# Kernel tuning notes

Hardware: AMD Instinct MI355X
Metric: run time of the kernel (lower is better)

## Reference

```python
import jax, jax.numpy as jnp
import numpy as np

PE_DIM = 64

def _layernorm(x, g, b, eps=1e-5):
    m = jnp.mean(x, -1, keepdims=True)
    v = jnp.mean((x - m) ** 2, -1, keepdims=True)
    return (x - m) * jax.lax.rsqrt(v + eps) * g + b

def _sinusoidal_pe(t, dim=PE_DIM):
    half = dim // 2
    freqs = jnp.exp(-jnp.log(10000.0) * jnp.arange(half) / half).astype(t.dtype)
    ang = t[..., None] * freqs  # [..., half]
    return jnp.concatenate([jnp.sin(ang), jnp.cos(ang)], -1)

def _bilinear(feats, b, t, x, y):
    # feats [B,Wl,H,W,D]; b,t int32 [B,Q,Wl,M] (b broadcastable); x,y in [0,1]
    # matches torch grid_sample(mode=bilinear, padding_mode=border, align_corners=False)
    H, W = feats.shape[2], feats.shape[3]
    px = x * W - 0.5
    py = y * H - 0.5
    x0 = jnp.floor(px); y0 = jnp.floor(py)
    wx = (px - x0)[..., None]; wy = (py - y0)[..., None]
    x0i = jnp.clip(x0.astype(jnp.int32), 0, W - 1)
    x1i = jnp.clip(x0.astype(jnp.int32) + 1, 0, W - 1)
    y0i = jnp.clip(y0.astype(jnp.int32), 0, H - 1)
    y1i = jnp.clip(y0.astype(jnp.int32) + 1, 0, H - 1)
    v00 = feats[b, t, y0i, x0i]  # [B,Q,Wl,M,D]
    v01 = feats[b, t, y0i, x1i]
    v10 = feats[b, t, y1i, x0i]
    v11 = feats[b, t, y1i, x1i]
    return (v00 * (1 - wy) * (1 - wx) + v01 * (1 - wy) * wx
            + v10 * wy * (1 - wx) + v11 * wy * wx)

def setup_inputs() -> dict:
    key = jax.random.key(0)
    ks = jax.random.split(key, 20)
    B, Q, Wl, H, W, D, M = 4, 300, 8, 64, 64, 256, 4
    s = 0.02
    inp = {
        'q': jax.random.normal(ks[0], (B, Q, D), jnp.float32),
        'kv_feats': jax.random.normal(ks[1], (B, Wl, H, W, D), jnp.float32),
        'kv_mask': jnp.zeros((B, Wl, H, W), jnp.bool_),
        'delta_sec': jax.random.normal(ks[2], (B, Q, Wl), jnp.float32),
        'w_ref': jax.random.normal(ks[3], (D, 2), jnp.float32) * s,
        'b_ref': jnp.zeros((2,), jnp.float32),
        'w_delta': jax.random.normal(ks[4], (2 * D, 3 * M), jnp.float32) * s,
        'b_delta': jnp.zeros((3 * M,), jnp.float32),
        'w_alpha': jax.random.normal(ks[5], (2 * D, M), jnp.float32) * s,
        'b_alpha': jnp.zeros((M,), jnp.float32),
        'lam': jnp.array(1.0, jnp.float32),
        'w_proj': jax.random.normal(ks[6], (D, D), jnp.float32) * s,
        'b_proj': jnp.zeros((D,), jnp.float32),
        'ln1_g': jnp.ones((D,), jnp.float32), 'ln1_b': jnp.zeros((D,), jnp.float32),
        'ln2_g': jnp.ones((D,), jnp.float32), 'ln2_b': jnp.zeros((D,), jnp.float32),
        'w_ffn1': jax.random.normal(ks[7], (D, 4 * D), jnp.float32) * s,
        'b_ffn1': jnp.zeros((4 * D,), jnp.float32),
        'w_ffn2': jax.random.normal(ks[8], (4 * D, D), jnp.float32) * s,
        'b_ffn2': jnp.zeros((D,), jnp.float32),
        'w_rel': jax.random.normal(ks[9], (PE_DIM, D), jnp.float32) * s,
        'b_rel': jnp.zeros((D,), jnp.float32),
    }
    return inp

def reference(q, kv_feats, kv_mask, delta_sec, w_ref, b_ref, w_delta, b_delta,
              w_alpha, b_alpha, lam, w_proj, b_proj, ln1_g, ln1_b, ln2_g, ln2_b,
              w_ffn1, b_ffn1, w_ffn2, b_ffn2, w_rel, b_rel):
    B, Q, D = q.shape
    Wl = kv_feats.shape[1]
    M = w_alpha.shape[1]

    qn = _layernorm(q, ln1_g, ln1_b)
    rel_feat = _sinusoidal_pe(delta_sec) @ w_rel + b_rel          # [B,Q,Wl,D]
    psi = jnp.concatenate([jnp.broadcast_to(qn[:, :, None, :], (B, Q, Wl, D)),
                           rel_feat], -1)                          # [B,Q,Wl,2D]

    delta = (psi @ w_delta + b_delta).reshape(B, Q, Wl, M, 3)
    logits = psi @ w_alpha + b_alpha                               # [B,Q,Wl,M]
    ref = jax.nn.sigmoid(qn @ w_ref + b_ref)                       # [B,Q,2]
    coords = ref[:, :, None, None, :] + jnp.tanh(delta[..., :2])   # [B,Q,Wl,M,2]
    coords = jnp.clip(coords, 0.0, 1.0)
    delta_t = jnp.tanh(delta[..., 2])                              # [B,Q,Wl,M]

    # mask features (mask==True -> invalid -> zero)
    feats = kv_feats * (~kv_mask)[..., None].astype(kv_feats.dtype)

    # temporal trilinear indices
    base = jnp.arange(Wl, dtype=q.dtype).reshape(1, 1, Wl, 1)
    target = base + delta_t
    t0f = jnp.clip(jnp.floor(target), 0, Wl - 1)
    t1f = jnp.clip(t0f + 1, 0, Wl - 1)
    alpha = (target - t0f)[..., None]
    t0 = t0f.astype(jnp.int32); t1 = t1f.astype(jnp.int32)

    bidx = jnp.arange(B, dtype=jnp.int32).reshape(B, 1, 1, 1)
    cx = coords[..., 0]; cy = coords[..., 1]
    s0 = _bilinear(feats, bidx, t0, cx, cy)                        # [B,Q,Wl,M,D]
    s1 = _bilinear(feats, bidx, t1, cx, cy)
    sampled = s0 * (1 - alpha) + s1 * alpha

    lam_sp = jax.nn.softplus(lam)
    weights = jax.nn.softmax(logits - lam_sp * jnp.abs(delta_sec)[..., None], axis=-1)
    agg = jnp.sum(weights[..., None] * sampled, axis=(2, 3))       # [B,Q,D]

    out = q + (agg @ w_proj + b_proj)
    h = _layernorm(out, ln2_g, ln2_b)
    ffn = jax.nn.gelu(h @ w_ffn1 + b_ffn1, approximate=False) @ w_ffn2 + b_ffn2
    return out + ffn
```

## Files before the change

### kernel.cpp

```cpp
#include <hip/hip_runtime.h>
#include <math.h>

#define Bn 4
#define Qn 300
#define WL 8
#define Hh 64
#define Ww 64
#define Dd 256
#define Mm 4

__device__ __forceinline__ float wave_reduce(float v) {
#pragma unroll
    for (int off = 32; off > 0; off >>= 1) v += __shfl_down(v, off, 64);
    return v;
}

__device__ __forceinline__ float block_reduce256(float v, float* lds) {
    v = wave_reduce(v);
    int lane = threadIdx.x & 63, wv = threadIdx.x >> 6;
    if (lane == 0) lds[wv] = v;
    __syncthreads();
    float r = lds[0] + lds[1] + lds[2] + lds[3];
    __syncthreads();
    return r;
}

__device__ __forceinline__ float lo16(unsigned u) { return __uint_as_float(u << 16); }
__device__ __forceinline__ float hi16(unsigned u) { return __uint_as_float(u & 0xffff0000u); }

__device__ __forceinline__ unsigned bfp(float a, float b) {
    unsigned ua = __float_as_uint(a); ua = (ua + 0x7fffu + ((ua >> 16) & 1u)) >> 16;
    unsigned ub = __float_as_uint(b); ub = (ub + 0x7fffu + ((ub >> 16) & 1u)) >> 16;
    return ua | (ub << 16);
}

__global__ void __launch_bounds__(256) k_pack(const float* __restrict__ wp,
                                              const float* __restrict__ wf1,
                                              const float* __restrict__ wf2,
                                              unsigned* __restrict__ pk) {
    int i = blockIdx.x * 256 + threadIdx.x;
    if (i < 32768) {
        int kk = i >> 8, c = i & 255;
        pk[i] = bfp(wp[(2 * kk) * 256 + c], wp[(2 * kk + 1) * 256 + c]);
    } else if (i < 163840) {
        int i2 = i - 32768; int kk = i2 >> 10, c = i2 & 1023;
        pk[i] = bfp(wf1[(2 * kk) * 1024 + c], wf1[(2 * kk + 1) * 1024 + c]);
    } else {
        int i3 = i - 163840; int kk = i3 >> 8, c = i3 & 255;
        pk[i] = bfp(wf2[(2 * kk) * 256 + c], wf2[(2 * kk + 1) * 256 + c]);
    }
}

__global__ void __launch_bounds__(256) k_mid(const float* __restrict__ q,
                                             const float* __restrict__ g1,
                                             const float* __restrict__ b1,
                                             const float* __restrict__ w_ref,
                                             const float* __restrict__ b_ref,
                                             const float* __restrict__ dsec,
                                             const float* __restrict__ w_rel,
                                             const float* __restrict__ b_rel,
                                             const float* __restrict__ w_delta,
                                             const float* __restrict__ b_delta,
                                             const float* __restrict__ w_alpha,
                                             const float* __restrict__ b_alpha,
                                             const unsigned char* __restrict__ mask,
                                             unsigned* __restrict__ prm2) {
    __shared__ float lds[4];
    __shared__ float sref[2];
    __shared__ float sqn[256];
    __shared__ float pe[8][64];
    __shared__ float rel[8][260];
    __shared__ float WcT[16 * 516];
    __shared__ float res[8][16];

    int bq = blockIdx.x, t = threadIdx.x;

    float x = q[bq * Dd + t];
    float m = block_reduce256(x, lds) * (1.f / Dd);
    float dx = x - m;
    float v = block_reduce256(dx * dx, lds) * (1.f / Dd);
    float y = dx * rsqrtf(v + 1e-5f) * g1[t] + b1[t];
    sqn[t] = y;

    float s0 = block_reduce256(y * w_ref[t * 2 + 0], lds);
    float s1 = block_reduce256(y * w_ref[t * 2 + 1], lds);
    if (t == 0) {
        sref[0] = 1.f / (1.f + expf(-(s0 + b_ref[0])));
        sref[1] = 1.f / (1.f + expf(-(s1 + b_ref[1])));
    }

    {
        int wl = t >> 5, i = t & 31;
        float f = expf(-logf(10000.f) * (float)i * (1.f / 32.f));
        float a = dsec[bq * WL + wl] * f;
        pe[wl][i] = sinf(a);
        pe[wl][i + 32] = cosf(a);
    }

    for (int u = t; u < 512 * 16; u += 256) {
        int k = u >> 4, jj = u & 15;
        float w = (jj < 12) ? w_delta[k * 12 + jj] : w_alpha[k * 4 + (jj - 12)];
        WcT[jj * 516 + k] = w;
    }

    float wr[64];
#pragma unroll
    for (int k = 0; k < 64; k++) wr[k] = w_rel[k * Dd + t];
    __syncthreads();

    float brl = b_rel[t];
    for (int wl = 0; wl < WL; wl++) {
        const float4* p4 = (const float4*)&pe[wl][0];
        float r = brl;
#pragma unroll
        for (int k4 = 0; k4 < 16; k4++) {
            float4 p = p4[k4];
            r += p.x * wr[4 * k4] + p.y * wr[4 * k4 + 1]
               + p.z * wr[4 * k4 + 2] + p.w * wr[4 * k4 + 3];
        }
        rel[wl][t] = r;
    }
    __syncthreads();

    if (t < 128) {
        int wl = t >> 4, jj = t & 15;
        const float4* wrow = (const float4*)&WcT[jj * 516];
        const float4* qrow = (const float4*)sqn;
        const float4* rrow = (const float4*)&rel[wl][0];
        float s = 0.f;
#pragma unroll 8
        for (int k4 = 0; k4 < 64; k4++) {
            float4 a = qrow[k4], w = wrow[k4];
            s += a.x * w.x + a.y * w.y + a.z * w.z + a.w * w.w;
        }
#pragma unroll 8
        for (int k4 = 0; k4 < 64; k4++) {
            float4 a = rrow[k4], w = wrow[64 + k4];
            s += a.x * w.x + a.y * w.y + a.z * w.z + a.w * w.w;
        }
        s += (jj < 12) ? b_delta[jj] : b_alpha[jj - 12];
        res[wl][jj] = s;
    }
    __syncthreads();

    if (t < 32) {
        int wl = t >> 2, mm = t & 3;
        float l0 = res[wl][12], l1 = res[wl][13], l2 = res[wl][14], l3 = res[wl][15];
        float mx = fmaxf(fmaxf(l0, l1), fmaxf(l2, l3));
        float inv = 1.f / (expf(l0 - mx) + expf(l1 - mx) + expf(l2 - mx) + expf(l3 - mx));
        float wgt = expf(res[wl][12 + mm] - mx) * inv;

        float cx = fminf(fmaxf(sref[0] + tanhf(res[wl][mm * 3 + 0]), 0.f), 1.f);
        float cy = fminf(fmaxf(sref[1] + tanhf(res[wl][mm * 3 + 1]), 0.f), 1.f);
        float tgt = (float)wl + tanhf(res[wl][mm * 3 + 2]);
        float t0f = fminf(fmaxf(floorf(tgt), 0.f), (float)(WL - 1));
        float t1f = fminf(t0f + 1.f, (float)(WL - 1));
        float alpha = tgt - t0f;
        float px = cx * (float)Ww - 0.5f, py = cy * (float)Hh - 0.5f;
        float fx = floorf(px), fy = floorf(py);
        float wx = px - fx, wy = py - fy;
        int X0 = (int)fminf(fmaxf(fx, 0.f), (float)(Ww - 1));
        int X1 = (int)fminf(fmaxf(fx + 1.f, 0.f), (float)(Ww - 1));
        int Y0 = (int)fminf(fmaxf(fy, 0.f), (float)(Hh - 1));
        int Y1 = (int)fminf(fmaxf(fy + 1.f, 0.f), (float)(Hh - 1));
        int T0 = (int)t0f, T1 = (int)t1f;

        float w00 = (1.f - wy) * (1.f - wx), w01 = (1.f - wy) * wx;
        float w10 = wy * (1.f - wx), w11 = wy * wx;
        float wt0 = wgt * (1.f - alpha), wt1 = wgt * alpha;

        int b = bq / Qn;
        int base0 = (b * WL + T0) * Hh;
        int base1 = (b * WL + T1) * Hh;
        int i00 = (base0 + Y0) * Ww + X0, i01 = (base0 + Y0) * Ww + X1;
        int i10 = (base0 + Y1) * Ww + X0, i11 = (base0 + Y1) * Ww + X1;
        int j00 = (base1 + Y0) * Ww + X0, j01 = (base1 + Y0) * Ww + X1;
        int j10 = (base1 + Y1) * Ww + X0, j11 = (base1 + Y1) * Ww + X1;

        unsigned* rec = prm2 + (unsigned)(bq * 32 + t) * 16;
        rec[0] = __float_as_uint(wt0 * w00 * (mask[i00] ? 0.f : 1.f));
        rec[1] = __float_as_uint(wt0 * w01 * (mask[i01] ? 0.f : 1.f));
        rec[2] = __float_as_uint(wt0 * w10 * (mask[i10] ? 0.f : 1.f));
        rec[3] = __float_as_uint(wt0 * w11 * (mask[i11] ? 0.f : 1.f));
        rec[4] = __float_as_uint(wt1 * w00 * (mask[j00] ? 0.f : 1.f));
        rec[5] = __float_as_uint(wt1 * w01 * (mask[j01] ? 0.f : 1.f));
        rec[6] = __float_as_uint(wt1 * w10 * (mask[j10] ? 0.f : 1.f));
        rec[7] = __float_as_uint(wt1 * w11 * (mask[j11] ? 0.f : 1.f));
        rec[8] = i00; rec[9] = i01; rec[10] = i10; rec[11] = i11;
        rec[12] = j00; rec[13] = j01; rec[14] = j10; rec[15] = j11;
    }
}

__global__ void __launch_bounds__(512) k_gather(const float* __restrict__ feats,
                                                const unsigned* __restrict__ prm2,
                                                float* __restrict__ agg) {
    __shared__ unsigned P[32 * 16];
    __shared__ float part[8][256];
    int bq = blockIdx.x, t = threadIdx.x;
    int l = t & 63, j = t >> 6;
    P[t] = prm2[(unsigned)bq * 512 + t];
    __syncthreads();
    const float4* f4 = (const float4*)feats;
    float4 acc = {0.f, 0.f, 0.f, 0.f};
#pragma unroll
    for (int p = 0; p < 4; p++) {
        const unsigned* rec = &P[(j * 4 + p) * 16];
#pragma unroll
        for (int cn = 0; cn < 8; cn++) {
            float w = __uint_as_float(rec[cn]);
            size_t idx = rec[8 + cn];
            float4 v = f4[idx * 64 + l];
            acc.x += w * v.x; acc.y += w * v.y; acc.z += w * v.z; acc.w += w * v.w;
        }
    }
    ((float4*)&part[j][0])[l] = acc;
    __syncthreads();
    if (t < 256) {
        float s = part[0][t] + part[1][t] + part[2][t] + part[3][t]
                + part[4][t] + part[5][t] + part[6][t] + part[7][t];
        agg[(size_t)bq * Dd + t] = s;
    }
}

template<int R>
__device__ __forceinline__ void out_body(int row0,
        const float* __restrict__ q, const float* __restrict__ agg,
        const unsigned* __restrict__ pkP, const float* __restrict__ b_proj,
        const float* __restrict__ g2, const float* __restrict__ b2,
        const unsigned* __restrict__ pkF1, const float* __restrict__ b_ffn1,
        const unsigned* __restrict__ pkF2, const float* __restrict__ b_ffn2,
        float* __restrict__ out,
        float* sA, float* sO, float* sH, float* sF, float* sP, float* sRed) {
    int t = threadIdx.x;
    int c = t & 255, j = t >> 8;

    for (int u = t; u < 256 * R; u += 1024) {
        int r = u >> 8, cc = u & 255;
        sA[r * 256 + cc] = agg[(size_t)(row0 + r) * Dd + cc];
    }
    __syncthreads();

    {
        float acc[R];
#pragma unroll
        for (int r = 0; r < R; r++) acc[r] = 0.f;
        const unsigned* wp = pkP + (j * 32) * 256 + c;
#pragma unroll 4
        for (int q4 = 0; q4 < 16; q4++) {
            unsigned u0 = wp[(2 * q4) * 256];
            unsigned u1 = wp[(2 * q4 + 1) * 256];
            float w0 = lo16(u0), w1 = hi16(u0), w2 = lo16(u1), w3 = hi16(u1);
#pragma unroll
            for (int r = 0; r < R; r++) {
                float4 a = ((const float4*)&sA[r * 256 + j * 64])[q4];
                acc[r] += a.x * w0 + a.y * w1 + a.z * w2 + a.w * w3;
            }
        }
#pragma unroll
        for (int r = 0; r < R; r++) sP[(j * 5 + r) * 256 + c] = acc[r];
    }
    __syncthreads();

    for (int u = t; u < 256 * R; u += 1024) {
        int r = u >> 8, cc = u & 255;
        float o = sP[(0 * 5 + r) * 256 + cc] + sP[(1 * 5 + r) * 256 + cc]
                + sP[(2 * 5 + r) * 256 + cc] + sP[(3 * 5 + r) * 256 + cc]
                + q[(size_t)(row0 + r) * Dd + cc] + b_proj[cc];
        sO[r * 256 + cc] = o;
    }
    __syncthreads();

    {
        int wv = t >> 6, l = t & 63;
        if (wv < R) {
            float4 v = ((const float4*)&sO[wv * 256])[l];
            float s = v.x + v.y + v.z + v.w;
            s = __shfl(wave_reduce(s), 0, 64);
            float mean = s * (1.f / 256.f);
            float d0 = v.x - mean, d1 = v.y - mean, d2 = v.z - mean, d3 = v.w - mean;
            float ss = d0 * d0 + d1 * d1 + d2 * d2 + d3 * d3;
            ss = __shfl(wave_reduce(ss), 0, 64);
            float rstd = rsqrtf(ss * (1.f / 256.f) + 1e-5f);
            if (l == 0) { sRed[wv * 2] = mean; sRed[wv * 2 + 1] = rstd; }
        }
    }
    __syncthreads();
    for (int u = t; u < 256 * R; u += 1024) {
        int r = u >> 8, cc = u & 255;
        sH[r * 256 + cc] = (sO[r * 256 + cc] - sRed[r * 2]) * sRed[r * 2 + 1] * g2[cc] + b2[cc];
    }
    __syncthreads();

    {
        float f[R];
#pragma unroll
        for (int r = 0; r < R; r++) f[r] = 0.f;
        const unsigned* wp = pkF1 + t;
#pragma unroll 4
        for (int q4 = 0; q4 < 64; q4++) {
            unsigned u0 = wp[(2 * q4) * 1024];
            unsigned u1 = wp[(2 * q4 + 1) * 1024];
            float w0 = lo16(u0), w1 = hi16(u0), w2 = lo16(u1), w3 = hi16(u1);
#pragma unroll
            for (int r = 0; r < R; r++) {
                float4 h = ((const float4*)&sH[r * 256])[q4];
                f[r] += h.x * w0 + h.y * w1 + h.z * w2 + h.w * w3;
            }
        }
        float bf = b_ffn1[t];
#pragma unroll
        for (int r = 0; r < R; r++) {
            float xx = f[r] + bf;
            sF[r * 1024 + t] = 0.5f * xx * (1.f + erff(xx * 0.70710678118654752f));
        }
    }
    __syncthreads();

    {
        float acc[R];
#pragma unroll
        for (int r = 0; r < R; r++) acc[r] = 0.f;
        const unsigned* wp = pkF2 + (j * 128) * 256 + c;
#pragma unroll 4
        for (int q4 = 0; q4 < 64; q4++) {
            unsigned u0 = wp[(2 * q4) * 256];
            unsigned u1 = wp[(2 * q4 + 1) * 256];
            float w0 = lo16(u0), w1 = hi16(u0), w2 = lo16(u1), w3 = hi16(u1);
#pragma unroll
            for (int r = 0; r < R; r++) {
                float4 h = ((const float4*)&sF[r * 1024 + j * 256])[q4];
                acc[r] += h.x * w0 + h.y * w1 + h.z * w2 + h.w * w3;
            }
        }
#pragma unroll
        for (int r = 0; r < R; r++) sP[(j * 5 + r) * 256 + c] = acc[r];
    }
    __syncthreads();

    for (int u = t; u < 256 * R; u += 1024) {
        int r = u >> 8, cc = u & 255;
        float s = sP[(0 * 5 + r) * 256 + cc] + sP[(1 * 5 + r) * 256 + cc]
                + sP[(2 * 5 + r) * 256 + cc] + sP[(3 * 5 + r) * 256 + cc];
        out[(size_t)(row0 + r) * Dd + cc] = sO[r * 256 + cc] + s + b_ffn2[cc];
    }
}

__global__ void __launch_bounds__(1024) k_out(const float* __restrict__ q,
                                              const float* __restrict__ agg,
                                              const unsigned* __restrict__ pkP,
                                              const float* __restrict__ b_proj,
                                              const float* __restrict__ g2,
                                              const float* __restrict__ b2,
                                              const unsigned* __restrict__ pkF1,
                                              const float* __restrict__ b_ffn1,
                                              const unsigned* __restrict__ pkF2,
                                              const float* __restrict__ b_ffn2,
                                              float* __restrict__ out) {
    __shared__ float sA[5 * 256];
    __shared__ float sO[5 * 256];
    __shared__ float sH[5 * 256];
    __shared__ float sF[5 * 1024];
    __shared__ float sP[4 * 5 * 256];
    __shared__ float sRed[16];
    __shared__ float pad[8192];
    if (b_ffn2 == nullptr) pad[threadIdx.x] = 0.f;

    int bid = blockIdx.x;
    if (bid < 176) {
        out_body<5>(bid * 5, q, agg, pkP, b_proj, g2, b2, pkF1, b_ffn1, pkF2, b_ffn2,
                    out, sA, sO, sH, sF, sP, sRed);
    } else {
        out_body<4>(880 + (bid - 176) * 4, q, agg, pkP, b_proj, g2, b2, pkF1, b_ffn1,
                    pkF2, b_ffn2, out, sA, sO, sH, sF, sP, sRed);
    }
}

extern "C" void kernel_launch(void* const* d_in, const int* in_sizes, int n_in,
                              void* d_out, int out_size, void* d_ws, size_t ws_size,
                              hipStream_t stream) {
    const float* q        = (const float*)d_in[0];
    const float* kv_feats = (const float*)d_in[1];
    const unsigned char* kv_mask = (const unsigned char*)d_in[2];
    const float* delta_sec= (const float*)d_in[3];
    const float* w_ref    = (const float*)d_in[4];
    const float* b_ref    = (const float*)d_in[5];
    const float* w_delta  = (const float*)d_in[6];
    const float* b_delta  = (const float*)d_in[7];
    const float* w_alpha  = (const float*)d_in[8];
    const float* b_alpha  = (const float*)d_in[9];
    const float* w_proj   = (const float*)d_in[11];
    const float* b_proj   = (const float*)d_in[12];
    const float* ln1_g    = (const float*)d_in[13];
    const float* ln1_b    = (const float*)d_in[14];
    const float* ln2_g    = (const float*)d_in[15];
    const float* ln2_b    = (const float*)d_in[16];
    const float* w_ffn1   = (const float*)d_in[17];
    const float* b_ffn1   = (const float*)d_in[18];
    const float* w_ffn2   = (const float*)d_in[19];
    const float* b_ffn2   = (const float*)d_in[20];
    const float* w_rel    = (const float*)d_in[21];
    const float* b_rel    = (const float*)d_in[22];
    float* out = (float*)d_out;

    unsigned* pk   = (unsigned*)d_ws;
    unsigned* pkP  = pk;
    unsigned* pkF1 = pk + 32768;
    unsigned* pkF2 = pk + 163840;
    unsigned* prm2 = pk + 294912;
    float*    agg  = (float*)(pk + 294912 + 614400);

    const int BQ = Bn * Qn;
    k_pack<<<dim3(1152), dim3(256), 0, stream>>>(w_proj, w_ffn1, w_ffn2, pk);
    k_mid<<<dim3(BQ), dim3(256), 0, stream>>>(q, ln1_g, ln1_b, w_ref, b_ref, delta_sec,
                                              w_rel, b_rel, w_delta, b_delta,
                                              w_alpha, b_alpha, kv_mask, prm2);
    k_gather<<<dim3(BQ), dim3(512), 0, stream>>>(kv_feats, prm2, agg);
    k_out<<<dim3(256), dim3(1024), 0, stream>>>(q, agg, pkP, b_proj, ln2_g, ln2_b,
                                                pkF1, b_ffn1, pkF2, b_ffn2, out);
}
```

Before: 307.9 us.

## Pre-transpose small weights in prep kernel and repack bf16 weights for wide loads

Folds the transposes of w_rel and the delta/alpha weights, plus the positional encoding, into the prep kernel so k_mid reads contiguous global arrays instead of rebuilding them per block. k_mid's 16-output projection is split across all 256 threads in chunks rather than using only 128. The bf16 weight packing is regrouped so each thread loads uint4 vectors covering 8 k-values for 4 columns. The out-kernel GEMMs then run on 256 of the 1024 threads, each with more register accumulators. This aims to cut redundant per-block transposes and widen weight loads, but it leaves three quarters of k_out's threads idle during the matmuls.

```diff
diff --git a/kernel.cpp b/kernel.cpp
--- a/kernel.cpp
+++ b/kernel.cpp
@@ -34,20 +34,47 @@
     return ua | (ub << 16);
 }
 
-__global__ void __launch_bounds__(256) k_pack(const float* __restrict__ wp,
+__global__ void __launch_bounds__(256) k_prep(const float* __restrict__ wp,
                                               const float* __restrict__ wf1,
                                               const float* __restrict__ wf2,
-                                              unsigned* __restrict__ pk) {
-    int i = blockIdx.x * 256 + threadIdx.x;
-    if (i < 32768) {
-        int kk = i >> 8, c = i & 255;
-        pk[i] = bfp(wp[(2 * kk) * 256 + c], wp[(2 * kk + 1) * 256 + c]);
-    } else if (i < 163840) {
-        int i2 = i - 32768; int kk = i2 >> 10, c = i2 & 1023;
-        pk[i] = bfp(wf1[(2 * kk) * 1024 + c], wf1[(2 * kk + 1) * 1024 + c]);
+                                              const float* __restrict__ w_rel,
+                                              const float* __restrict__ dsec,
+                                              const float* __restrict__ w_delta,
+                                              const float* __restrict__ w_alpha,
+                                              unsigned* __restrict__ pk,
+                                              float* __restrict__ wrT,
+                                              float* __restrict__ WcTg,
+                                              float* __restrict__ peg) {
+    int bid = blockIdx.x, t = threadIdx.x;
+    if (bid < 1152) {
+        int i = bid * 256 + t;
+        if (i < 32768) {
+            int p = i & 3, c = (i >> 2) & 255, g = i >> 10;
+            pk[i] = bfp(wp[(g * 8 + 2 * p) * 256 + c], wp[(g * 8 + 2 * p + 1) * 256 + c]);
+        } else if (i < 163840) {
+            int i2 = i - 32768;
+            int p = i2 & 3, c = (i2 >> 2) & 1023, g = i2 >> 12;
+            pk[i] = bfp(wf1[(g * 8 + 2 * p) * 1024 + c], wf1[(g * 8 + 2 * p + 1) * 1024 + c]);
+        } else {
+            int i3 = i - 163840;
+            int p = i3 & 3, c = (i3 >> 2) & 255, g = i3 >> 10;
+            pk[i] = bfp(wf2[(g * 8 + 2 * p) * 256 + c], wf2[(g * 8 + 2 * p + 1) * 256 + c]);
+        }
+    } else if (bid < 1216) {
+        int u = (bid - 1152) * 256 + t;
+        int col = u >> 6, k = u & 63;
+        wrT[u] = w_rel[k * 256 + col];
+    } else if (bid < 1248) {
+        int u = (bid - 1216) * 256 + t;
+        int jj = u >> 9, k = u & 511;
+        WcTg[u] = (jj < 12) ? w_delta[k * 12 + jj] : w_alpha[k * 4 + (jj - 12)];
     } else {
-        int i3 = i - 163840; int kk = i3 >> 8, c = i3 & 255;
-        pk[i] = bfp(wf2[(2 * kk) * 256 + c], wf2[(2 * kk + 1) * 256 + c]);
+        int bq = bid - 1248;
+        int wl = t >> 5, i = t & 31;
+        float f = expf(-logf(10000.f) * (float)i * (1.f / 32.f));
+        float a = dsec[bq * WL + wl] * f;
+        peg[bq * 512 + wl * 64 + i] = sinf(a);
+        peg[bq * 512 + wl * 64 + 32 + i] = cosf(a);
     }
 }
 
@@ -56,21 +83,20 @@
                                              const float* __restrict__ b1,
                                              const float* __restrict__ w_ref,
                                              const float* __restrict__ b_ref,
-                                             const float* __restrict__ dsec,
-                                             const float* __restrict__ w_rel,
+                                             const float* __restrict__ wrT,
+                                             const float* __restrict__ WcTg,
+                                             const float* __restrict__ peg,
                                              const float* __restrict__ b_rel,
-                                             const float* __restrict__ w_delta,
                                              const float* __restrict__ b_delta,
-                                             const float* __restrict__ w_alpha,
                                              const float* __restrict__ b_alpha,
                                              const unsigned char* __restrict__ mask,
                                              unsigned* __restrict__ prm2) {
     __shared__ float lds[4];
     __shared__ float sref[2];
     __shared__ float sqn[256];
-    __shared__ float pe[8][64];
-    __shared__ float rel[8][260];
-    __shared__ float WcT[16 * 516];
+    __shared__ float relS[8][260];
+    __shared__ float qpart[8][16];
+    __shared__ float rp[8][8][16];
     __shared__ float res[8][16];
 
     int bq = blockIdx.x, t = threadIdx.x;
@@ -89,56 +115,75 @@
         sref[1] = 1.f / (1.f + expf(-(s1 + b_ref[1])));
     }
 
+    float wr[64];
     {
-        int wl = t >> 5, i = t & 31;
-        float f = expf(-logf(10000.f) * (float)i * (1.f / 32.f));
-        float a = dsec[bq * WL + wl] * f;
-        pe[wl][i] = sinf(a);
-        pe[wl][i + 32] = cosf(a);
-    }
-
-    for (int u = t; u < 512 * 16; u += 256) {
-        int k = u >> 4, jj = u & 15;
-        float w = (jj < 12) ? w_delta[k * 12 + jj] : w_alpha[k * 4 + (jj - 12)];
-        WcT[jj * 516 + k] = w;
-    }
-
-    float wr[64];
-#pragma unroll
-    for (int k = 0; k < 64; k++) wr[k] = w_rel[k * Dd + t];
-    __syncthreads();
-
-    float brl = b_rel[t];
-    for (int wl = 0; wl < WL; wl++) {
-        const float4* p4 = (const float4*)&pe[wl][0];
-        float r = brl;
-#pragma unroll
-        for (int k4 = 0; k4 < 16; k4++) {
-            float4 p = p4[k4];
-            r += p.x * wr[4 * k4] + p.y * wr[4 * k4 + 1]
-               + p.z * wr[4 * k4 + 2] + p.w * wr[4 * k4 + 3];
-        }
-        rel[wl][t] = r;
-    }
-    __syncthreads();
-
+        const float4* w4 = (const float4*)&wrT[t * 64];
+#pragma unroll
+        for (int i = 0; i < 16; i++) {
+            float4 vv = w4[i];
+            wr[4 * i] = vv.x; wr[4 * i + 1] = vv.y; wr[4 * i + 2] = vv.z; wr[4 * i + 3] = vv.w;
+        }
+    }
+
+    {
+        const float* pg = peg + bq * 512;
+        float brl = b_rel[t];
+#pragma unroll
+        for (int wl = 0; wl < WL; wl++) {
+            const float4* p4 = (const float4*)(pg + wl * 64);
+            float r = brl;
+#pragma unroll
+            for (int k4 = 0; k4 < 16; k4++) {
+                float4 p = p4[k4];
+                r += p.x * wr[4 * k4] + p.y * wr[4 * k4 + 1]
+                   + p.z * wr[4 * k4 + 2] + p.w * wr[4 * k4 + 3];
+            }
+            relS[wl][t] = r;
+        }
+    }
+    __syncthreads();
+
+    {
+        int chunk = t >> 4, jj = t & 15;
+        float w[32];
+        const float4* wg = (const float4*)&WcTg[jj * 512 + chunk * 32];
+#pragma unroll
+        for (int i = 0; i < 8; i++) {
+            float4 vv = wg[i];
+            w[4 * i] = vv.x; w[4 * i + 1] = vv.y; w[4 * i + 2] = vv.z; w[4 * i + 3] = vv.w;
+        }
+        if (chunk < 8) {
+            const float4* a4 = (const float4*)&sqn[chunk * 32];
+            float s = 0.f;
+#pragma unroll
+            for (int ii = 0; ii < 8; ii++) {
+                int i = (ii + chunk) & 7;
+                float4 a = a4[i];
+                s += a.x * w[4 * i] + a.y * w[4 * i + 1] + a.z * w[4 * i + 2] + a.w * w[4 * i + 3];
+            }
+            qpart[chunk][jj] = s;
+        } else {
+            int ch = chunk - 8;
+#pragma unroll
+            for (int wl = 0; wl < WL; wl++) {
+                const float4* a4 = (const float4*)&relS[wl][ch * 32];
+                float s = 0.f;
+#pragma unroll
+                for (int ii = 0; ii < 8; ii++) {
+                    int i = (ii + ch) & 7;
+                    float4 a = a4[i];
+                    s += a.x * w[4 * i] + a.y * w[4 * i + 1] + a.z * w[4 * i + 2] + a.w * w[4 * i + 3];
+                }
+                rp[wl][ch][jj] = s;
+            }
+        }
+    }
+    __syncthreads();
     if (t < 128) {
         int wl = t >> 4, jj = t & 15;
-        const float4* wrow = (const float4*)&WcT[jj * 516];
-        const float4* qrow = (const float4*)sqn;
-        const float4* rrow = (const float4*)&rel[wl][0];
-        float s = 0.f;
-#pragma unroll 8
-        for (int k4 = 0; k4 < 64; k4++) {
-            float4 a = qrow[k4], w = wrow[k4];
-            s += a.x * w.x + a.y * w.y + a.z * w.z + a.w * w.w;
-        }
-#pragma unroll 8
-        for (int k4 = 0; k4 < 64; k4++) {
-            float4 a = rrow[k4], w = wrow[64 + k4];
-            s += a.x * w.x + a.y * w.y + a.z * w.z + a.w * w.w;
-        }
-        s += (jj < 12) ? b_delta[jj] : b_alpha[jj - 12];
+        float s = (jj < 12) ? b_delta[jj] : b_alpha[jj - 12];
+#pragma unroll
+        for (int c = 0; c < 8; c++) s += qpart[c][jj] + rp[wl][c][jj];
         res[wl][jj] = s;
     }
     __syncthreads();
@@ -232,7 +277,6 @@
         float* __restrict__ out,
         float* sA, float* sO, float* sH, float* sF, float* sP, float* sRed) {
     int t = threadIdx.x;
-    int c = t & 255, j = t >> 8;
 
     for (int u = t; u < 256 * R; u += 1024) {
         int r = u >> 8, cc = u & 255;
@@ -240,24 +284,44 @@
     }
     __syncthreads();
 
-    {
-        float acc[R];
-#pragma unroll
-        for (int r = 0; r < R; r++) acc[r] = 0.f;
-        const unsigned* wp = pkP + (j * 32) * 256 + c;
-#pragma unroll 4
-        for (int q4 = 0; q4 < 16; q4++) {
-            unsigned u0 = wp[(2 * q4) * 256];
-            unsigned u1 = wp[(2 * q4 + 1) * 256];
-            float w0 = lo16(u0), w1 = hi16(u0), w2 = lo16(u1), w3 = hi16(u1);
+    if (t < 256) {
+        int j = t >> 6, cq = t & 63;
+        float acc[R][4];
+#pragma unroll
+        for (int r = 0; r < R; r++)
+#pragma unroll
+            for (int cc = 0; cc < 4; cc++) acc[r][cc] = 0.f;
+#pragma unroll 2
+        for (int gg = 0; gg < 8; gg++) {
+            int g = j * 8 + gg;
+            uint4 wv[4];
+#pragma unroll
+            for (int cc = 0; cc < 4; cc++)
+                wv[cc] = *(const uint4*)&pkP[((g * 256) + cq + 64 * cc) * 4];
+            float4 ha[R], hb[R];
 #pragma unroll
             for (int r = 0; r < R; r++) {
-                float4 a = ((const float4*)&sA[r * 256 + j * 64])[q4];
-                acc[r] += a.x * w0 + a.y * w1 + a.z * w2 + a.w * w3;
-            }
-        }
-#pragma unroll
-        for (int r = 0; r < R; r++) sP[(j * 5 + r) * 256 + c] = acc[r];
+                ha[r] = ((const float4*)&sA[r * 256])[g * 2];
+                hb[r] = ((const float4*)&sA[r * 256])[g * 2 + 1];
+            }
+#pragma unroll
+            for (int cc = 0; cc < 4; cc++) {
+                float w0 = lo16(wv[cc].x), w1 = hi16(wv[cc].x);
+                float w2 = lo16(wv[cc].y), w3 = hi16(wv[cc].y);
+                float w4 = lo16(wv[cc].z), w5 = hi16(wv[cc].z);
+                float w6 = lo16(wv[cc].w), w7 = hi16(wv[cc].w);
+#pragma unroll
+                for (int r = 0; r < R; r++) {
+                    acc[r][cc] += ha[r].x * w0 + ha[r].y * w1 + ha[r].z * w2 + ha[r].w * w3
+                                + hb[r].x * w4 + hb[r].y * w5 + hb[r].z * w6 + hb[r].w * w7;
+                }
+            }
+        }
+#pragma unroll
+        for (int r = 0; r < R; r++)
+#pragma unroll
+            for (int cc = 0; cc < 4; cc++)
+                sP[(j * 5 + r) * 256 + cq + 64 * cc] = acc[r][cc];
     }
     __syncthreads();
 
@@ -291,49 +355,88 @@
     }
     __syncthreads();
 
-    {
-        float f[R];
-#pragma unroll
-        for (int r = 0; r < R; r++) f[r] = 0.f;
-        const unsigned* wp = pkF1 + t;
-#pragma unroll 4
-        for (int q4 = 0; q4 < 64; q4++) {
-            unsigned u0 = wp[(2 * q4) * 1024];
-            unsigned u1 = wp[(2 * q4 + 1) * 1024];
-            float w0 = lo16(u0), w1 = hi16(u0), w2 = lo16(u1), w3 = hi16(u1);
+    if (t < 256) {
+        float f[R][4];
+#pragma unroll
+        for (int r = 0; r < R; r++)
+#pragma unroll
+            for (int cc = 0; cc < 4; cc++) f[r][cc] = 0.f;
+#pragma unroll 2
+        for (int g = 0; g < 32; g++) {
+            uint4 wv[4];
+#pragma unroll
+            for (int cc = 0; cc < 4; cc++)
+                wv[cc] = *(const uint4*)&pkF1[((g * 1024) + t + 256 * cc) * 4];
+            float4 ha[R], hb[R];
 #pragma unroll
             for (int r = 0; r < R; r++) {
-                float4 h = ((const float4*)&sH[r * 256])[q4];
-                f[r] += h.x * w0 + h.y * w1 + h.z * w2 + h.w * w3;
-            }
-        }
-        float bf = b_ffn1[t];
-#pragma unroll
-        for (int r = 0; r < R; r++) {
-            float xx = f[r] + bf;
-            sF[r * 1024 + t] = 0.5f * xx * (1.f + erff(xx * 0.70710678118654752f));
-        }
-    }
-    __syncthreads();
-
-    {
-        float acc[R];
-#pragma unroll
-        for (int r = 0; r < R; r++) acc[r] = 0.f;
-        const unsigned* wp = pkF2 + (j * 128) * 256 + c;
-#pragma unroll 4
-        for (int q4 = 0; q4 < 64; q4++) {
-            unsigned u0 = wp[(2 * q4) * 256];
-            unsigned u1 = wp[(2 * q4 + 1) * 256];
-            float w0 = lo16(u0), w1 = hi16(u0), w2 = lo16(u1), w3 = hi16(u1);
+                ha[r] = ((const float4*)&sH[r * 256])[g * 2];
+                hb[r] = ((const float4*)&sH[r * 256])[g * 2 + 1];
+            }
+#pragma unroll
+            for (int cc = 0; cc < 4; cc++) {
+                float w0 = lo16(wv[cc].x), w1 = hi16(wv[cc].x);
+                float w2 = lo16(wv[cc].y), w3 = hi16(wv[cc].y);
+                float w4 = lo16(wv[cc].z), w5 = hi16(wv[cc].z);
+                float w6 = lo16(wv[cc].w), w7 = hi16(wv[cc].w);
+#pragma unroll
+                for (int r = 0; r < R; r++) {
+                    f[r][cc] += ha[r].x * w0 + ha[r].y * w1 + ha[r].z * w2 + ha[r].w * w3
+                              + hb[r].x * w4 + hb[r].y * w5 + hb[r].z * w6 + hb[r].w * w7;
+                }
+            }
+        }
+#pragma unroll
+        for (int cc = 0; cc < 4; cc++) {
+            int col = t + 256 * cc;
+            float bf = b_ffn1[col];
 #pragma unroll
             for (int r = 0; r < R; r++) {
-                float4 h = ((const float4*)&sF[r * 1024 + j * 256])[q4];
-                acc[r] += h.x * w0 + h.y * w1 + h.z * w2 + h.w * w3;
-            }
-        }
-#pragma unroll
-        for (int r = 0; r < R; r++) sP[(j * 5 + r) * 256 + c] = acc[r];
+                float xx = f[r][cc] + bf;
+                sF[r * 1024 + col] = 0.5f * xx * (1.f + erff(xx * 0.70710678118654752f));
+            }
+        }
+    }
+    __syncthreads();
+
+    if (t < 256) {
+        int j = t >> 6, cq = t & 63;
+        float acc[R][4];
+#pragma unroll
+        for (int r = 0; r < R; r++)
+#pragma unroll
+            for (int cc = 0; cc < 4; cc++) acc[r][cc] = 0.f;
+#pragma unroll 2
+        for (int gg = 0; gg < 32; gg++) {
+            int g = j * 32 + gg;
+            uint4 wv[4];
+#pragma unroll
+            for (int cc = 0; cc < 4; cc++)
+                wv[cc] = *(const uint4*)&pkF2[((g * 256) + cq + 64 * cc) * 4];
+            float4 ha[R], hb[R];
+#pragma unroll
+            for (int r = 0; r < R; r++) {
+                ha[r] = ((const float4*)&sF[r * 1024])[g * 2];
+                hb[r] = ((const float4*)&sF[r * 1024])[g * 2 + 1];
+            }
+#pragma unroll
+            for (int cc = 0; cc < 4; cc++) {
+                float w0 = lo16(wv[cc].x), w1 = hi16(wv[cc].x);
+                float w2 = lo16(wv[cc].y), w3 = hi16(wv[cc].y);
+                float w4 = lo16(wv[cc].z), w5 = hi16(wv[cc].z);
+                float w6 = lo16(wv[cc].w), w7 = hi16(wv[cc].w);
+#pragma unroll
+                for (int r = 0; r < R; r++) {
+                    acc[r][cc] += ha[r].x * w0 + ha[r].y * w1 + ha[r].z * w2 + ha[r].w * w3
+                                + hb[r].x * w4 + hb[r].y * w5 + hb[r].z * w6 + hb[r].w * w7;
+                }
+            }
+        }
+#pragma unroll
+        for (int r = 0; r < R; r++)
+#pragma unroll
+            for (int cc = 0; cc < 4; cc++)
+                sP[(j * 5 + r) * 256 + cq + 64 * cc] = acc[r][cc];
     }
     __syncthreads();
 
@@ -406,14 +509,19 @@
     unsigned* pkP  = pk;
     unsigned* pkF1 = pk + 32768;
     unsigned* pkF2 = pk + 163840;
-    unsigned* prm2 = pk + 294912;
-    float*    agg  = (float*)(pk + 294912 + 614400);
+    float*    wrT  = (float*)(pk + 294912);
+    float*    WcTg = wrT + 16384;
+    float*    peg  = WcTg + 8192;
+    unsigned* prm2 = (unsigned*)(peg + 614400);
+    float*    agg  = (float*)(prm2 + 614400);
 
     const int BQ = Bn * Qn;
-    k_pack<<<dim3(1152), dim3(256), 0, stream>>>(w_proj, w_ffn1, w_ffn2, pk);
-    k_mid<<<dim3(BQ), dim3(256), 0, stream>>>(q, ln1_g, ln1_b, w_ref, b_ref, delta_sec,
-                                              w_rel, b_rel, w_delta, b_delta,
-                                              w_alpha, b_alpha, kv_mask, prm2);
+    k_prep<<<dim3(1248 + BQ), dim3(256), 0, stream>>>(w_proj, w_ffn1, w_ffn2, w_rel,
+                                                      delta_sec, w_delta, w_alpha,
+                                                      pk, wrT, WcTg, peg);
+    k_mid<<<dim3(BQ), dim3(256), 0, stream>>>(q, ln1_g, ln1_b, w_ref, b_ref,
+                                              wrT, WcTg, peg, b_rel,
+                                              b_delta, b_alpha, kv_mask, prm2);
     k_gather<<<dim3(BQ), dim3(512), 0, stream>>>(kv_feats, prm2, agg);
     k_out<<<dim3(256), dim3(1024), 0, stream>>>(q, agg, pkP, b_proj, ln2_g, ln2_b,
                                                 pkF1, b_ffn1, pkF2, b_ffn2, out);
```

Measured after the change: 314.0 us. About the same (+2.0%).

## Fold weight packing into k_mid and repack bf16 weights for 16-byte loads

Applied to the files above, without the earlier changes.

The separate bf16 weight-packing kernel is merged into k_mid as extra leading blocks, which removes one kernel launch. The packed layout is also changed so that each thread's eight consecutive K-values for one output column sit contiguously. The three GEMM loops in the output stage can then fetch them with a single uint4 load instead of two strided 32-bit loads. In exchange, k_mid's LDS-heavy block shape now covers the trivial packing blocks, and the wider per-thread loads may change coalescing patterns.

```diff
diff --git a/kernel.cpp b/kernel.cpp
--- a/kernel.cpp
+++ b/kernel.cpp
@@ -34,24 +34,11 @@
     return ua | (ub << 16);
 }
 
-__global__ void __launch_bounds__(256) k_pack(const float* __restrict__ wp,
-                                              const float* __restrict__ wf1,
-                                              const float* __restrict__ wf2,
-                                              unsigned* __restrict__ pk) {
-    int i = blockIdx.x * 256 + threadIdx.x;
-    if (i < 32768) {
-        int kk = i >> 8, c = i & 255;
-        pk[i] = bfp(wp[(2 * kk) * 256 + c], wp[(2 * kk + 1) * 256 + c]);
-    } else if (i < 163840) {
-        int i2 = i - 32768; int kk = i2 >> 10, c = i2 & 1023;
-        pk[i] = bfp(wf1[(2 * kk) * 1024 + c], wf1[(2 * kk + 1) * 1024 + c]);
-    } else {
-        int i3 = i - 163840; int kk = i3 >> 8, c = i3 & 255;
-        pk[i] = bfp(wf2[(2 * kk) * 256 + c], wf2[(2 * kk + 1) * 256 + c]);
-    }
-}
-
-__global__ void __launch_bounds__(256) k_mid(const float* __restrict__ q,
+__global__ void __launch_bounds__(256) k_mid(const float* __restrict__ wp,
+                                             const float* __restrict__ wf1,
+                                             const float* __restrict__ wf2,
+                                             unsigned* __restrict__ pk,
+                                             const float* __restrict__ q,
                                              const float* __restrict__ g1,
                                              const float* __restrict__ b1,
                                              const float* __restrict__ w_ref,
@@ -73,7 +60,26 @@
     __shared__ float WcT[16 * 516];
     __shared__ float res[8][16];
 
-    int bq = blockIdx.x, t = threadIdx.x;
+    int bid = blockIdx.x, t = threadIdx.x;
+
+    if (bid < 1152) {
+        int i = bid * 256 + t;
+        if (i < 32768) {
+            int p = i & 3, c = (i >> 2) & 255, g = i >> 10;
+            pk[i] = bfp(wp[(g * 8 + 2 * p) * 256 + c], wp[(g * 8 + 2 * p + 1) * 256 + c]);
+        } else if (i < 163840) {
+            int i2 = i - 32768;
+            int p = i2 & 3, c = (i2 >> 2) & 1023, g = i2 >> 12;
+            pk[i] = bfp(wf1[(g * 8 + 2 * p) * 1024 + c], wf1[(g * 8 + 2 * p + 1) * 1024 + c]);
+        } else {
+            int i3 = i - 163840;
+            int p = i3 & 3, c = (i3 >> 2) & 255, g = i3 >> 10;
+            pk[i] = bfp(wf2[(g * 8 + 2 * p) * 256 + c], wf2[(g * 8 + 2 * p + 1) * 256 + c]);
+        }
+        return;
+    }
+
+    int bq = bid - 1152;
 
     float x = q[bq * Dd + t];
     float m = block_reduce256(x, lds) * (1.f / Dd);
@@ -244,16 +250,18 @@
         float acc[R];
 #pragma unroll
         for (int r = 0; r < R; r++) acc[r] = 0.f;
-        const unsigned* wp = pkP + (j * 32) * 256 + c;
-#pragma unroll 4
-        for (int q4 = 0; q4 < 16; q4++) {
-            unsigned u0 = wp[(2 * q4) * 256];
-            unsigned u1 = wp[(2 * q4 + 1) * 256];
-            float w0 = lo16(u0), w1 = hi16(u0), w2 = lo16(u1), w3 = hi16(u1);
+#pragma unroll 2
+        for (int gg = 0; gg < 8; gg++) {
+            int g = j * 8 + gg;
+            uint4 wv = *(const uint4*)&pkP[((unsigned)(g * 256 + c)) * 4];
+            float w0 = lo16(wv.x), w1 = hi16(wv.x), w2 = lo16(wv.y), w3 = hi16(wv.y);
+            float w4 = lo16(wv.z), w5 = hi16(wv.z), w6 = lo16(wv.w), w7 = hi16(wv.w);
 #pragma unroll
             for (int r = 0; r < R; r++) {
-                float4 a = ((const float4*)&sA[r * 256 + j * 64])[q4];
-                acc[r] += a.x * w0 + a.y * w1 + a.z * w2 + a.w * w3;
+                float4 ha = ((const float4*)&sA[r * 256])[g * 2];
+                float4 hb = ((const float4*)&sA[r * 256])[g * 2 + 1];
+                acc[r] += ha.x * w0 + ha.y * w1 + ha.z * w2 + ha.w * w3
+                        + hb.x * w4 + hb.y * w5 + hb.z * w6 + hb.w * w7;
             }
         }
 #pragma unroll
@@ -295,16 +303,17 @@
         float f[R];
 #pragma unroll
         for (int r = 0; r < R; r++) f[r] = 0.f;
-        const unsigned* wp = pkF1 + t;
-#pragma unroll 4
-        for (int q4 = 0; q4 < 64; q4++) {
-            unsigned u0 = wp[(2 * q4) * 1024];
-            unsigned u1 = wp[(2 * q4 + 1) * 1024];
-            float w0 = lo16(u0), w1 = hi16(u0), w2 = lo16(u1), w3 = hi16(u1);
+#pragma unroll 2
+        for (int g = 0; g < 32; g++) {
+            uint4 wv = *(const uint4*)&pkF1[((unsigned)(g * 1024 + t)) * 4];
+            float w0 = lo16(wv.x), w1 = hi16(wv.x), w2 = lo16(wv.y), w3 = hi16(wv.y);
+            float w4 = lo16(wv.z), w5 = hi16(wv.z), w6 = lo16(wv.w), w7 = hi16(wv.w);
 #pragma unroll
             for (int r = 0; r < R; r++) {
-                float4 h = ((const float4*)&sH[r * 256])[q4];
-                f[r] += h.x * w0 + h.y * w1 + h.z * w2 + h.w * w3;
+                float4 ha = ((const float4*)&sH[r * 256])[g * 2];
+                float4 hb = ((const float4*)&sH[r * 256])[g * 2 + 1];
+                f[r] += ha.x * w0 + ha.y * w1 + ha.z * w2 + ha.w * w3
+                      + hb.x * w4 + hb.y * w5 + hb.z * w6 + hb.w * w7;
             }
         }
         float bf = b_ffn1[t];
@@ -320,16 +329,18 @@
         float acc[R];
 #pragma unroll
         for (int r = 0; r < R; r++) acc[r] = 0.f;
-        const unsigned* wp = pkF2 + (j * 128) * 256 + c;
-#pragma unroll 4
-        for (int q4 = 0; q4 < 64; q4++) {
-            unsigned u0 = wp[(2 * q4) * 256];
-            unsigned u1 = wp[(2 * q4 + 1) * 256];
-            float w0 = lo16(u0), w1 = hi16(u0), w2 = lo16(u1), w3 = hi16(u1);
+#pragma unroll 2
+        for (int gg = 0; gg < 32; gg++) {
+            int g = j * 32 + gg;
+            uint4 wv = *(const uint4*)&pkF2[((unsigned)(g * 256 + c)) * 4];
+            float w0 = lo16(wv.x), w1 = hi16(wv.x), w2 = lo16(wv.y), w3 = hi16(wv.y);
+            float w4 = lo16(wv.z), w5 = hi16(wv.z), w6 = lo16(wv.w), w7 = hi16(wv.w);
 #pragma unroll
             for (int r = 0; r < R; r++) {
-                float4 h = ((const float4*)&sF[r * 1024 + j * 256])[q4];
-                acc[r] += h.x * w0 + h.y * w1 + h.z * w2 + h.w * w3;
+                float4 ha = ((const float4*)&sF[r * 1024])[g * 2];
+                float4 hb = ((const float4*)&sF[r * 1024])[g * 2 + 1];
+                acc[r] += ha.x * w0 + ha.y * w1 + ha.z * w2 + ha.w * w3
+                        + hb.x * w4 + hb.y * w5 + hb.z * w6 + hb.w * w7;
             }
         }
 #pragma unroll
@@ -407,13 +418,14 @@
     unsigned* pkF1 = pk + 32768;
     unsigned* pkF2 = pk + 163840;
     unsigned* prm2 = pk + 294912;
-    float*    agg  = (float*)(pk + 294912 + 614400);
+    float*    agg  = (float*)(prm2 + 614400);
 
     const int BQ = Bn * Qn;
-    k_pack<<<dim3(1152), dim3(256), 0, stream>>>(w_proj, w_ffn1, w_ffn2, pk);
-    k_mid<<<dim3(BQ), dim3(256), 0, stream>>>(q, ln1_g, ln1_b, w_ref, b_ref, delta_sec,
-                                              w_rel, b_rel, w_delta, b_delta,
-                                              w_alpha, b_alpha, kv_mask, prm2);
+    k_mid<<<dim3(1152 + BQ), dim3(256), 0, stream>>>(w_proj, w_ffn1, w_ffn2, pk,
+                                                     q, ln1_g, ln1_b, w_ref, b_ref,
+                                                     delta_sec, w_rel, b_rel,
+                                                     w_delta, b_delta, w_alpha, b_alpha,
+                                                     kv_mask, prm2);
     k_gather<<<dim3(BQ), dim3(512), 0, stream>>>(kv_feats, prm2, agg);
     k_out<<<dim3(256), dim3(1024), 0, stream>>>(q, agg, pkP, b_proj, ln2_g, ln2_b,
                                                 pkF1, b_ffn1, pkF2, b_ffn2, out);
```

New measurement: 300.0 us. -2.5%, faster.
